# Optimization experiments

Hardware: AMD Instinct MI355X
Metric: run time of the kernel (lower is better)

Reference implementation:

```python
import jax, jax.numpy as jnp
import numpy as np

BLOCK = 256
H, D = 16, 128          # num_attention_heads, head_dim
HID = 2048              # hidden_size (= H*D)
FFN = 2048              # intermediate_size
E, TOPK = 8, 2          # num_local_experts, num_experts_per_tok
EPS_LN = 1e-5           # rms_norm_eps for layer norms
EPS_ATTN = float(np.finfo(np.float32).eps)  # torch RMSNorm default eps


def rmsnorm(x, w, eps):
    v = jnp.mean(jnp.square(x), axis=-1, keepdims=True)
    return x * jax.lax.rsqrt(v + eps) * w


def lightning_attn(x, slope, qkv_w, gate_w, norm_w, out_w):
    # x: [B,N,HID]; slope: [H,1,1]
    B, N, _ = x.shape
    qkv = jax.nn.silu(x @ qkv_w.T).reshape(B, N, H, 3 * D)
    q, k, v = jnp.split(qkv, 3, axis=-1)
    q = q.transpose(0, 2, 1, 3)  # [B,H,N,D]
    k = k.transpose(0, 2, 1, 3)
    v = v.transpose(0, 2, 1, 3)

    NB = N // BLOCK
    ar = jnp.arange(BLOCK, dtype=jnp.float32) + 1.0
    q_decay = jnp.exp(-slope * ar[:, None])             # [H,BLOCK,1]
    k_decay = jnp.exp(-slope * (BLOCK - ar[:, None]))   # [H,BLOCK,1]
    idx = ar[:, None] - ar[None, :]                      # [BLOCK,BLOCK]
    diag_decay = jnp.exp(jnp.where(idx >= 0, -(slope * idx), -jnp.inf))  # [H,BLOCK,BLOCK]
    block_decay = jnp.exp(-slope * BLOCK)                # [H,1,1]

    qb = q.reshape(B, H, NB, BLOCK, D).transpose(2, 0, 1, 3, 4)  # [NB,B,H,BLOCK,D]
    kb = k.reshape(B, H, NB, BLOCK, D).transpose(2, 0, 1, 3, 4)
    vb = v.reshape(B, H, NB, BLOCK, D).transpose(2, 0, 1, 3, 4)

    def step(kv, blk):
        qi, ki, vi = blk                                   # [B,H,BLOCK,D]
        o_nd = jnp.einsum('bhmd,bhde->bhme', qi * q_decay, kv)
        qk = jnp.einsum('bhmd,bhnd->bhmn', qi, ki) * diag_decay[None]
        o_d = jnp.einsum('bhmn,bhne->bhme', qk, vi)
        kv = block_decay * kv + jnp.einsum('bhmd,bhme->bhde', ki * k_decay, vi)
        return kv, o_nd + o_d

    kv0 = jnp.zeros((B, H, D, D), jnp.float32)
    _, out = jax.lax.scan(step, kv0, (qb, kb, vb))         # out: [NB,B,H,BLOCK,D]
    out = out.transpose(1, 2, 0, 3, 4).reshape(B, H, N, D)
    out = out.transpose(0, 2, 1, 3).reshape(B, N, H * D)   # b h n d -> b n (h d)
    out = rmsnorm(out, norm_w, EPS_ATTN)
    out = jax.nn.sigmoid(x @ gate_w.T) * out
    return out @ out_w.T


def moe(x, router_w, w1, w2, w3):
    # x: [B,N,HID]
    B, N, _ = x.shape
    xt = x.reshape(B * N, HID)                             # [T,HID]
    T = B * N
    logits = xt @ router_w.T                               # [T,E]
    probs = jax.nn.softmax(logits.astype(jnp.float32), axis=-1)
    w, sel = jax.lax.top_k(probs, TOPK)                    # [T,TOPK]
    w = w / jnp.sum(w, axis=-1, keepdims=True)
    w = w.astype(xt.dtype)
    # dense combine weights [T,E] (top-k experts are distinct)
    cw = jnp.zeros((T, E), xt.dtype).at[jnp.arange(T)[:, None], sel].add(w)
    h1 = jax.nn.silu(jnp.einsum('td,efd->tef', xt, w1))    # [T,E,FFN]
    h3 = jnp.einsum('td,efd->tef', xt, w3)
    ye = jnp.einsum('tef,edf->ted', h1 * h3, w2)           # [T,E,HID]
    out = jnp.einsum('te,ted->td', cw, ye)
    return out.reshape(B, N, HID)


def setup_inputs() -> dict:
    key = jax.random.key(0)
    ks = jax.random.split(key, 12)
    s = 0.02
    B, N = 1, 1024
    x = jax.random.normal(ks[0], (B, N, HID), jnp.float32)
    # ALiBi-like positive per-head decay rates
    slope_rate = (1.0 / (2.0 ** (8.0 * (jnp.arange(H, dtype=jnp.float32) + 1) / H))).reshape(H, 1, 1)
    return {
        'x': x,
        'slope_rate': slope_rate,
        'ln1_w': jnp.ones((HID,), jnp.float32),
        'ln2_w': jnp.ones((HID,), jnp.float32),
        'qkv_w': jax.random.normal(ks[1], (3 * H * D, HID), jnp.float32) * s,
        'ogate_w': jax.random.normal(ks[2], (H * D, HID), jnp.float32) * s,
        'anorm_w': jnp.ones((H * D,), jnp.float32),
        'aout_w': jax.random.normal(ks[3], (HID, H * D), jnp.float32) * s,
        'router_w': jax.random.normal(ks[4], (E, HID), jnp.float32) * s,
        'w1': jax.random.normal(ks[5], (E, FFN, HID), jnp.float32) * s,
        'w2': jax.random.normal(ks[6], (E, HID, FFN), jnp.float32) * s,
        'w3': jax.random.normal(ks[7], (E, FFN, HID), jnp.float32) * s,
    }


def reference(x, slope_rate, ln1_w, ln2_w, qkv_w, ogate_w, anorm_w, aout_w, router_w, w1, w2, w3):
    # pre-norm residual decoder layer (alpha=beta=1, postnorm=False, no shared MoE)
    r = x
    h = rmsnorm(x, ln1_w, EPS_LN)
    h = r + lightning_attn(h, slope_rate, qkv_w, ogate_w, anorm_w, aout_w)
    r = h
    h2 = rmsnorm(h, ln2_w, EPS_LN)
    return r + moe(h2, router_w, w1, w2, w3)
```

## Files before the change

kernel.cpp:

```cpp
#include <hip/hip_runtime.h>
#include <math.h>

#define NTOK 1024
#define NHID 2048
#define NQKV 6144
#define NHEADS 16
#define DHEAD 128
#define ABLK 256
#define NEXPERT 8
#define NFFN 2048
#define EPS_LN 1e-5f
#define EPS_ATTN 1.1920929e-7f

typedef __bf16 bf8v __attribute__((ext_vector_type(8)));
typedef __bf16 bf4v __attribute__((ext_vector_type(4)));
typedef float f4v __attribute__((ext_vector_type(4)));

static __device__ __forceinline__ f4v mfma16(bf8v a, bf8v b, f4v c) {
  return __builtin_amdgcn_mfma_f32_16x16x32_bf16(a, b, c, 0, 0, 0);
}

static __device__ __forceinline__ void gl2lds16(const float* g, float* l) {
  __builtin_amdgcn_global_load_lds(
      (const __attribute__((address_space(1))) float*)g,
      (__attribute__((address_space(3))) float*)l, 16, 0, 0);
}

__global__ __launch_bounds__(256) void rms_kernel(const float* __restrict__ in,
                                                  const float* __restrict__ w,
                                                  float* __restrict__ out,
                                                  const float* __restrict__ gate,
                                                  float* __restrict__ copy_out,
                                                  float eps) {
  const int row = blockIdx.x, tid = threadIdx.x;
  const float* p = in + (size_t)row * NHID;
  float4 v0 = *(const float4*)(p + 4 * tid);
  float4 v1 = *(const float4*)(p + 1024 + 4 * tid);
  float ss = v0.x * v0.x + v0.y * v0.y + v0.z * v0.z + v0.w * v0.w
           + v1.x * v1.x + v1.y * v1.y + v1.z * v1.z + v1.w * v1.w;
  for (int off = 32; off > 0; off >>= 1) ss += __shfl_down(ss, off);
  __shared__ float red[4];
  const int wv = tid >> 6, ln = tid & 63;
  if (ln == 0) red[wv] = ss;
  __syncthreads();
  const float tot = red[0] + red[1] + red[2] + red[3];
  const float rinv = rsqrtf(tot * (1.f / NHID) + eps);
  float4 w0 = *(const float4*)(w + 4 * tid);
  float4 w1 = *(const float4*)(w + 1024 + 4 * tid);
  float4 o0, o1;
  o0.x = v0.x * rinv * w0.x; o0.y = v0.y * rinv * w0.y;
  o0.z = v0.z * rinv * w0.z; o0.w = v0.w * rinv * w0.w;
  o1.x = v1.x * rinv * w1.x; o1.y = v1.y * rinv * w1.y;
  o1.z = v1.z * rinv * w1.z; o1.w = v1.w * rinv * w1.w;
  if (gate) {
    const float* gp = gate + (size_t)row * NHID;
    float4 g0 = *(const float4*)(gp + 4 * tid);
    float4 g1 = *(const float4*)(gp + 1024 + 4 * tid);
    o0.x *= g0.x; o0.y *= g0.y; o0.z *= g0.z; o0.w *= g0.w;
    o1.x *= g1.x; o1.y *= g1.y; o1.z *= g1.z; o1.w *= g1.w;
  }
  *(float4*)(out + (size_t)row * NHID + 4 * tid) = o0;
  *(float4*)(out + (size_t)row * NHID + 1024 + 4 * tid) = o1;
  if (copy_out) {
    *(float4*)(copy_out + (size_t)row * NHID + 4 * tid) = v0;
    *(float4*)(copy_out + (size_t)row * NHID + 1024 + 4 * tid) = v1;
  }
}

enum { GM_QKV = 0, GM_GATE = 1, GM_AOUT = 2, GM_MOE1 = 3, GM_MOE3 = 4, GM_MOE2 = 5 };

struct GArgs {
  const float* A; const float* B; float* C;
  const float* res;
  float* q_s; float* k_s; float* v_s;
  const int* perm; const int* segoff; const float* pw;
  float* outp;
  int N, K;
};

template <int MODE>
__global__ __launch_bounds__(256, 2) void gemm_bt(GArgs g) {
  const int n0 = blockIdx.x * 64;
  const int m0 = blockIdx.y * 128;
  int segbase = 0, cnt = 0x40000000, e = 0;
  if constexpr (MODE >= GM_MOE1) {
    e = blockIdx.z;
    segbase = g.segoff[e];
    cnt = g.segoff[e + 1] - segbase;
    if (m0 >= cnt) return;
  }
  const float* Bp = g.B + (size_t)e * g.N * g.K + (size_t)n0 * g.K;
  __shared__ float As[128 * 32];
  __shared__ float Bs[64 * 32];
  const int tid = threadIdx.x;
  const int w = tid >> 6, lane = tid & 63;
  const int wm = (w >> 1) * 64, wn = (w & 1) * 32;
  const int lm = lane & 15, quad = lane >> 4;
  const int lr = lane >> 3;
  const int coff = ((lane & 7) ^ lr) * 4;
  const int K = g.K;

  const float* aptr[4];
  const float* bptr[2];
#pragma unroll
  for (int qi = 0; qi < 4; qi++) {
    const int r = (w * 4 + qi) * 8 + lr;
    const int m = m0 + r;
    long grow;
    if constexpr (MODE == GM_MOE1 || MODE == GM_MOE3) {
      int mm = m < cnt ? m : cnt - 1;
      grow = g.perm[segbase + mm];
    } else if constexpr (MODE == GM_MOE2) {
      grow = segbase + (m < cnt ? m : cnt - 1);
    } else {
      grow = m;
    }
    aptr[qi] = g.A + (size_t)grow * K + coff;
  }
#pragma unroll
  for (int qi = 0; qi < 2; qi++) {
    const int r = (w * 2 + qi) * 8 + lr;
    bptr[qi] = Bp + (size_t)r * K + coff;
  }

  const f4v fz = {0.f, 0.f, 0.f, 0.f};
  f4v acc[4][2];
#pragma unroll
  for (int i = 0; i < 4; i++) {
    acc[i][0] = fz; acc[i][1] = fz;
  }

  for (int k0 = 0; k0 < K; k0 += 32) {
    __syncthreads();
#pragma unroll
    for (int qi = 0; qi < 4; qi++)
      gl2lds16(aptr[qi] + k0, &As[(w * 4 + qi) * 256]);
#pragma unroll
    for (int qi = 0; qi < 2; qi++)
      gl2lds16(bptr[qi] + k0, &Bs[(w * 2 + qi) * 256]);
    __syncthreads();
    bf8v af[4], bfv[2];
    const int sw = lm & 7;
#pragma unroll
    for (int i = 0; i < 4; i++) {
      const int ra = wm + i * 16 + lm;
      const float4 x0 = *(const float4*)&As[ra * 32 + (((quad * 2) ^ sw) << 2)];
      const float4 x1 = *(const float4*)&As[ra * 32 + (((quad * 2 + 1) ^ sw) << 2)];
      bf8v t;
      t[0] = (__bf16)x0.x; t[1] = (__bf16)x0.y; t[2] = (__bf16)x0.z; t[3] = (__bf16)x0.w;
      t[4] = (__bf16)x1.x; t[5] = (__bf16)x1.y; t[6] = (__bf16)x1.z; t[7] = (__bf16)x1.w;
      af[i] = t;
    }
#pragma unroll
    for (int j = 0; j < 2; j++) {
      const int rb = wn + j * 16 + lm;
      const float4 x0 = *(const float4*)&Bs[rb * 32 + (((quad * 2) ^ sw) << 2)];
      const float4 x1 = *(const float4*)&Bs[rb * 32 + (((quad * 2 + 1) ^ sw) << 2)];
      bf8v t;
      t[0] = (__bf16)x0.x; t[1] = (__bf16)x0.y; t[2] = (__bf16)x0.z; t[3] = (__bf16)x0.w;
      t[4] = (__bf16)x1.x; t[5] = (__bf16)x1.y; t[6] = (__bf16)x1.z; t[7] = (__bf16)x1.w;
      bfv[j] = t;
    }
#pragma unroll
    for (int i = 0; i < 4; i++)
#pragma unroll
      for (int j = 0; j < 2; j++) acc[i][j] = mfma16(af[i], bfv[j], acc[i][j]);
  }

#pragma unroll
  for (int i = 0; i < 4; i++) {
#pragma unroll
    for (int r = 0; r < 4; r++) {
      const int m = m0 + wm + i * 16 + quad * 4 + r;
      int tok = 0;
      float wgt = 0.f;
      if constexpr (MODE == GM_MOE2) {
        if (m < cnt) { tok = g.perm[segbase + m]; wgt = g.pw[segbase + m]; }
      }
#pragma unroll
      for (int j = 0; j < 2; j++) {
        const int col = n0 + wn + j * 16 + lm;
        float v = acc[i][j][r];
        if constexpr (MODE == GM_QKV) {
          v = v / (1.f + expf(-v));
          int head = col / 384;
          int rem = col - head * 384;
          int which = rem >> 7;
          int d = rem & 127;
          float* dst = which == 0 ? g.q_s : (which == 1 ? g.k_s : g.v_s);
          dst[((size_t)head * NTOK + m) * DHEAD + d] = v;
        } else if constexpr (MODE == GM_GATE) {
          g.C[(size_t)m * g.N + col] = 1.f / (1.f + expf(-v));
        } else if constexpr (MODE == GM_AOUT) {
          g.C[(size_t)m * g.N + col] = v + g.res[(size_t)m * g.N + col];
        } else if constexpr (MODE == GM_MOE1) {
          if (m < cnt) g.C[(size_t)(segbase + m) * g.N + col] = v / (1.f + expf(-v));
        } else if constexpr (MODE == GM_MOE3) {
          if (m < cnt) {
            size_t ix = (size_t)(segbase + m) * g.N + col;
            g.C[ix] = v * g.res[ix];
          }
        } else if constexpr (MODE == GM_MOE2) {
          if (m < cnt) atomicAdd(&g.outp[(size_t)tok * NHID + col], wgt * v);
        }
      }
    }
  }
}

__global__ __launch_bounds__(512) void attn_pass1(const float* __restrict__ k_s,
                                                  const float* __restrict__ v_s,
                                                  const float* __restrict__ slope,
                                                  float* __restrict__ S) {
  const int h = blockIdx.x >> 2, b = blockIdx.x & 3;
  const float s = slope[h];
  __shared__ __bf16 kT[128][40] __attribute__((aligned(16)));
  __shared__ __bf16 vT[128][40] __attribute__((aligned(16)));
  const int tid = threadIdx.x, wave = tid >> 6, lane = tid & 63;
  const int lm = lane & 15, quad = lane >> 4;
  const float* kb = k_s + ((size_t)h * NTOK + b * ABLK) * DHEAD;
  const float* vb = v_s + ((size_t)h * NTOK + b * ABLK) * DHEAD;
  const int sd = tid & 127, sg = (tid >> 7) * 8;
  const f4v fz = {0.f, 0.f, 0.f, 0.f};
  f4v acc[8];
#pragma unroll
  for (int j = 0; j < 8; j++) acc[j] = fz;
  for (int ic = 0; ic < 8; ic++) {
    __syncthreads();
    bf8v kq, vq;
#pragma unroll
    for (int ii = 0; ii < 8; ii++) {
      int ig = ic * 32 + sg + ii;
      float kd = expf(-s * (float)(ABLK - 1 - ig));
      kq[ii] = (__bf16)(kb[(size_t)ig * DHEAD + sd] * kd);
      vq[ii] = (__bf16)(vb[(size_t)ig * DHEAD + sd]);
    }
    *(bf8v*)&kT[sd][sg] = kq;
    *(bf8v*)&vT[sd][sg] = vq;
    __syncthreads();
    bf8v a = *(const bf8v*)&kT[wave * 16 + lm][quad * 8];
#pragma unroll
    for (int j = 0; j < 8; j++) {
      bf8v bb = *(const bf8v*)&vT[j * 16 + lm][quad * 8];
      acc[j] = mfma16(a, bb, acc[j]);
    }
  }
  float* Sp = S + (size_t)(h * 4 + b) * (128 * 128);
#pragma unroll
  for (int j = 0; j < 8; j++)
#pragma unroll
    for (int r = 0; r < 4; r++)
      Sp[(size_t)(wave * 16 + quad * 4 + r) * 128 + j * 16 + lm] = acc[j][r];
}

__global__ __launch_bounds__(512) void attn_pass2(const float* __restrict__ q_s,
                                                  const float* __restrict__ k_s,
                                                  const float* __restrict__ v_s,
                                                  const float* __restrict__ slope,
                                                  const float* __restrict__ S,
                                                  float* __restrict__ attn_raw) {
  const int h = blockIdx.x >> 2, b = blockIdx.x & 3;
  const float s = slope[h];
  __shared__ __bf16 kvb[128][136] __attribute__((aligned(16)));
  __shared__ __bf16 vT[128][40] __attribute__((aligned(16)));
  __shared__ __bf16 ki[32][136] __attribute__((aligned(16)));
  __shared__ __bf16 qkb[256][40] __attribute__((aligned(16)));
  const int tid = threadIdx.x, w = tid >> 6, lane = tid & 63;
  const int lm = lane & 15, quad = lane >> 4;
  {
    const int sd = tid >> 2;
    const int e0 = (tid & 3) * 32;
    float vals[32];
#pragma unroll
    for (int u = 0; u < 32; u++) vals[u] = 0.f;
    for (int j = 0; j < b; j++) {
      float c = expf(-s * 256.f * (float)(b - 1 - j));
      const float* Sp = S + (size_t)(h * 4 + j) * (128 * 128) + (size_t)sd * 128 + e0;
#pragma unroll
      for (int u4 = 0; u4 < 8; u4++) {
        float4 sv = *(const float4*)(Sp + u4 * 4);
        vals[u4 * 4 + 0] += c * sv.x; vals[u4 * 4 + 1] += c * sv.y;
        vals[u4 * 4 + 2] += c * sv.z; vals[u4 * 4 + 3] += c * sv.w;
      }
    }
#pragma unroll
    for (int u = 0; u < 32; u++) kvb[e0 + u][sd] = (__bf16)vals[u];
  }
  __syncthreads();
  const float* qb = q_s + ((size_t)h * NTOK + b * ABLK) * DHEAD;
  const float* kb = k_s + ((size_t)h * NTOK + b * ABLK) * DHEAD;
  const float* vb = v_s + ((size_t)h * NTOK + b * ABLK) * DHEAD;
  bf8v aq[2][4];
#pragma unroll
  for (int mf = 0; mf < 2; mf++) {
    const int m = w * 32 + mf * 16 + lm;
#pragma unroll
    for (int kc = 0; kc < 4; kc++) {
      const float* pp = qb + (size_t)m * DHEAD + kc * 32 + quad * 8;
      float4 u0 = *(const float4*)pp;
      float4 u1 = *(const float4*)(pp + 4);
      bf8v t;
      t[0] = (__bf16)u0.x; t[1] = (__bf16)u0.y; t[2] = (__bf16)u0.z; t[3] = (__bf16)u0.w;
      t[4] = (__bf16)u1.x; t[5] = (__bf16)u1.y; t[6] = (__bf16)u1.z; t[7] = (__bf16)u1.w;
      aq[mf][kc] = t;
    }
  }
  const f4v fz = {0.f, 0.f, 0.f, 0.f};
  f4v accO[2][8];
#pragma unroll
  for (int mf = 0; mf < 2; mf++)
#pragma unroll
    for (int nf = 0; nf < 8; nf++) accO[mf][nf] = fz;
#pragma unroll
  for (int kc = 0; kc < 4; kc++) {
#pragma unroll
    for (int nf = 0; nf < 8; nf++) {
      bf8v bb = *(const bf8v*)&kvb[nf * 16 + lm][kc * 32 + quad * 8];
      accO[0][nf] = mfma16(aq[0][kc], bb, accO[0][nf]);
      accO[1][nf] = mfma16(aq[1][kc], bb, accO[1][nf]);
    }
  }
#pragma unroll
  for (int mf = 0; mf < 2; mf++) {
#pragma unroll
    for (int r = 0; r < 4; r++) {
      const int m = w * 32 + mf * 16 + quad * 4 + r;
      const float qd = expf(-s * (float)(m + 1));
#pragma unroll
      for (int nf = 0; nf < 8; nf++) accO[mf][nf][r] *= qd;
    }
  }
  for (int ic = 0; ic < 8; ic++) {
    __syncthreads();
    {
      const int si = tid >> 4, dc = (tid & 15) * 8;
      const float* pp = kb + (size_t)(ic * 32 + si) * DHEAD + dc;
      float4 u0 = *(const float4*)pp;
      float4 u1 = *(const float4*)(pp + 4);
      bf8v t;
      t[0] = (__bf16)u0.x; t[1] = (__bf16)u0.y; t[2] = (__bf16)u0.z; t[3] = (__bf16)u0.w;
      t[4] = (__bf16)u1.x; t[5] = (__bf16)u1.y; t[6] = (__bf16)u1.z; t[7] = (__bf16)u1.w;
      *(bf8v*)&ki[si][dc] = t;
    }
    {
      const int se = tid & 127, sg = (tid >> 7) * 8;
      bf8v t;
#pragma unroll
      for (int ii = 0; ii < 8; ii++)
        t[ii] = (__bf16)vb[(size_t)(ic * 32 + sg + ii) * DHEAD + se];
      *(bf8v*)&vT[se][sg] = t;
    }
    __syncthreads();
    f4v acc2[2][2];
    acc2[0][0] = fz; acc2[0][1] = fz; acc2[1][0] = fz; acc2[1][1] = fz;
#pragma unroll
    for (int kc = 0; kc < 4; kc++) {
#pragma unroll
      for (int f = 0; f < 2; f++) {
        bf8v bk = *(const bf8v*)&ki[f * 16 + lm][kc * 32 + quad * 8];
        acc2[0][f] = mfma16(aq[0][kc], bk, acc2[0][f]);
        acc2[1][f] = mfma16(aq[1][kc], bk, acc2[1][f]);
      }
    }
#pragma unroll
    for (int mf = 0; mf < 2; mf++) {
#pragma unroll
      for (int f = 0; f < 2; f++) {
#pragma unroll
        for (int r = 0; r < 4; r++) {
          const int m = w * 32 + mf * 16 + quad * 4 + r;
          const int i = ic * 32 + f * 16 + lm;
          float v = acc2[mf][f][r];
          v = (m >= i) ? v * expf(-s * (float)(m - i)) : 0.f;
          qkb[m][f * 16 + lm] = (__bf16)v;
        }
      }
    }
    __syncthreads();
#pragma unroll
    for (int mf = 0; mf < 2; mf++) {
      bf8v aqk = *(const bf8v*)&qkb[w * 32 + mf * 16 + lm][quad * 8];
#pragma unroll
      for (int nf = 0; nf < 8; nf++) {
        bf8v bv = *(const bf8v*)&vT[nf * 16 + lm][quad * 8];
        accO[mf][nf] = mfma16(aqk, bv, accO[mf][nf]);
      }
    }
  }
  float* op = attn_raw + (size_t)(b * ABLK) * NHID + h * DHEAD;
#pragma unroll
  for (int mf = 0; mf < 2; mf++)
#pragma unroll
    for (int r = 0; r < 4; r++) {
      const int m = w * 32 + mf * 16 + quad * 4 + r;
#pragma unroll
      for (int nf = 0; nf < 8; nf++)
        op[(size_t)m * NHID + nf * 16 + lm] = accO[mf][nf][r];
    }
}

__global__ __launch_bounds__(256) void router_kernel(const float* __restrict__ h2,
                                                     const float* __restrict__ rw,
                                                     int* __restrict__ eidx,
                                                     float* __restrict__ ew) {
  const int wave = threadIdx.x >> 6, lane = threadIdx.x & 63;
  const int t = blockIdx.x * 4 + wave;
  float a[8];
#pragma unroll
  for (int e = 0; e < 8; e++) a[e] = 0.f;
  for (int d = lane; d < NHID; d += 64) {
    float xv = h2[(size_t)t * NHID + d];
#pragma unroll
    for (int e = 0; e < 8; e++) a[e] += xv * rw[(size_t)e * NHID + d];
  }
#pragma unroll
  for (int e = 0; e < 8; e++)
    for (int off = 32; off > 0; off >>= 1) a[e] += __shfl_down(a[e], off);
  if (lane == 0) {
    int i1 = 0;
#pragma unroll
    for (int e = 1; e < 8; e++)
      if (a[e] > a[i1]) i1 = e;
    int i2 = i1 == 0 ? 1 : 0;
#pragma unroll
    for (int e = 0; e < 8; e++) {
      if (e == i1 || e == i2) continue;
      if (a[e] > a[i2]) i2 = e;
    }
    float be = expf(a[i2] - a[i1]);
    float w1 = 1.f / (1.f + be), w2 = be / (1.f + be);
    eidx[2 * t] = i1; eidx[2 * t + 1] = i2;
    ew[2 * t] = w1; ew[2 * t + 1] = w2;
  }
}

__global__ __launch_bounds__(256) void build_lists(const int* __restrict__ eidx,
                                                   const float* __restrict__ ew,
                                                   int* __restrict__ segoff,
                                                   int* __restrict__ perm,
                                                   float* __restrict__ pw) {
  __shared__ int cnt[8], cur[8], offs[9];
  const int tid = threadIdx.x;
  if (tid < 8) cnt[tid] = 0;
  __syncthreads();
  for (int t = tid; t < NTOK; t += 256) {
    atomicAdd(&cnt[eidx[2 * t]], 1);
    atomicAdd(&cnt[eidx[2 * t + 1]], 1);
  }
  __syncthreads();
  if (tid == 0) {
    int o = 0;
    for (int e = 0; e < 8; e++) { offs[e] = o; o += cnt[e]; }
    offs[8] = o;
    for (int e = 0; e < 9; e++) segoff[e] = offs[e];
  }
  __syncthreads();
  if (tid < 8) cur[tid] = offs[tid];
  __syncthreads();
  for (int t = tid; t < NTOK; t += 256) {
    for (int k = 0; k < 2; k++) {
      int e = eidx[2 * t + k];
      int pos = atomicAdd(&cur[e], 1);
      perm[pos] = t;
      pw[pos] = ew[2 * t + k];
    }
  }
}

extern "C" void kernel_launch(void* const* d_in, const int* in_sizes, int n_in,
                              void* d_out, int out_size, void* d_ws, size_t ws_size,
                              hipStream_t stream) {
  (void)in_sizes; (void)n_in; (void)out_size; (void)ws_size;
  const float* x        = (const float*)d_in[0];
  const float* slope    = (const float*)d_in[1];
  const float* ln1_w    = (const float*)d_in[2];
  const float* ln2_w    = (const float*)d_in[3];
  const float* qkv_w    = (const float*)d_in[4];
  const float* ogate_w  = (const float*)d_in[5];
  const float* anorm_w  = (const float*)d_in[6];
  const float* aout_w   = (const float*)d_in[7];
  const float* router_w = (const float*)d_in[8];
  const float* w1       = (const float*)d_in[9];
  const float* w2       = (const float*)d_in[10];
  const float* w3       = (const float*)d_in[11];
  float* out = (float*)d_out;
  float* ws  = (float*)d_ws;

  const size_t MW = (size_t)NTOK * NHID;
  float* a_ln     = ws;
  float* q_s      = ws + MW;
  float* k_s      = ws + 2 * MW;
  float* v_s      = ws + 3 * MW;
  float* Sbuf     = ws + 4 * MW;
  float* attn_raw = ws + 4 * MW + MW / 2;
  float* gatebuf  = ws + 5 * MW + MW / 2;
  float* t1       = ws + 4 * MW + MW / 2;
  float* rbase    = ws + 6 * MW + MW / 2;
  int*   eidx   = (int*)rbase;
  float* ew     = rbase + 2048;
  int*   segoff = (int*)(rbase + 4096);
  int*   perm   = (int*)(rbase + 4112);
  float* pw     = rbase + 6160;
  float* h_res = k_s;
  float* h2    = v_s;
  float* ag    = a_ln;

  rms_kernel<<<dim3(NTOK), dim3(256), 0, stream>>>(x, ln1_w, a_ln, nullptr, nullptr, EPS_LN);
  {
    GArgs g{}; g.A = a_ln; g.B = qkv_w; g.q_s = q_s; g.k_s = k_s; g.v_s = v_s;
    g.N = NQKV; g.K = NHID;
    gemm_bt<GM_QKV><<<dim3(NQKV / 64, NTOK / 128), dim3(256), 0, stream>>>(g);
  }
  attn_pass1<<<dim3(64), dim3(512), 0, stream>>>(k_s, v_s, slope, Sbuf);
  attn_pass2<<<dim3(64), dim3(512), 0, stream>>>(q_s, k_s, v_s, slope, Sbuf, attn_raw);
  {
    GArgs g{}; g.A = a_ln; g.B = ogate_w; g.C = gatebuf; g.N = NHID; g.K = NHID;
    gemm_bt<GM_GATE><<<dim3(32, 8), dim3(256), 0, stream>>>(g);
  }
  rms_kernel<<<dim3(NTOK), dim3(256), 0, stream>>>(attn_raw, anorm_w, ag, gatebuf, nullptr, EPS_ATTN);
  {
    GArgs g{}; g.A = ag; g.B = aout_w; g.C = h_res; g.res = x; g.N = NHID; g.K = NHID;
    gemm_bt<GM_AOUT><<<dim3(32, 8), dim3(256), 0, stream>>>(g);
  }
  rms_kernel<<<dim3(NTOK), dim3(256), 0, stream>>>(h_res, ln2_w, h2, nullptr, out, EPS_LN);
  router_kernel<<<dim3(NTOK / 4), dim3(256), 0, stream>>>(h2, router_w, eidx, ew);
  build_lists<<<dim3(1), dim3(256), 0, stream>>>(eidx, ew, segoff, perm, pw);
  {
    GArgs g{}; g.A = h2; g.B = w1; g.C = t1; g.perm = perm; g.segoff = segoff;
    g.N = NFFN; g.K = NHID;
    gemm_bt<GM_MOE1><<<dim3(32, 16, 8), dim3(256), 0, stream>>>(g);
  }
  {
    GArgs g{}; g.A = h2; g.B = w3; g.C = t1; g.res = t1; g.perm = perm; g.segoff = segoff;
    g.N = NFFN; g.K = NHID;
    gemm_bt<GM_MOE3><<<dim3(32, 16, 8), dim3(256), 0, stream>>>(g);
  }
  {
    GArgs g{}; g.A = t1; g.B = w2; g.outp = out; g.perm = perm; g.segoff = segoff; g.pw = pw;
    g.N = NHID; g.K = NFFN;
    gemm_bt<GM_MOE2><<<dim3(32, 16, 8), dim3(256), 0, stream>>>(g);
  }
}
```

Measured before the change: 998.1 us.

## Double-buffer LDS tiles in gemm_bt to overlap global loads with MFMA

The GEMM main loop now uses two LDS buffers for the A and B tiles. It issues the async global-to-LDS loads for the next K-slice before converting and multiplying the current slice, and uses one barrier per iteration instead of two. Launch bounds are raised from 2 to 3 blocks per SM to allow more occupancy, which tightens the register budget and doubles the LDS footprint per block (48KB). The intent is to hide global load latency behind compute, at the risk of register spills or lower real occupancy.

```diff
diff --git a/kernel.cpp b/kernel.cpp
--- a/kernel.cpp
+++ b/kernel.cpp
@@ -79,7 +79,7 @@
 };
 
 template <int MODE>
-__global__ __launch_bounds__(256, 2) void gemm_bt(GArgs g) {
+__global__ __launch_bounds__(256, 3) void gemm_bt(GArgs g) {
   const int n0 = blockIdx.x * 64;
   const int m0 = blockIdx.y * 128;
   int segbase = 0, cnt = 0x40000000, e = 0;
@@ -90,8 +90,8 @@
     if (m0 >= cnt) return;
   }
   const float* Bp = g.B + (size_t)e * g.N * g.K + (size_t)n0 * g.K;
-  __shared__ float As[128 * 32];
-  __shared__ float Bs[64 * 32];
+  __shared__ float As[2][128 * 32];
+  __shared__ float Bs[2][64 * 32];
   const int tid = threadIdx.x;
   const int w = tid >> 6, lane = tid & 63;
   const int wm = (w >> 1) * 64, wn = (w & 1) * 32;
@@ -130,41 +130,53 @@
     acc[i][0] = fz; acc[i][1] = fz;
   }
 
-  for (int k0 = 0; k0 < K; k0 += 32) {
-    __syncthreads();
-#pragma unroll
-    for (int qi = 0; qi < 4; qi++)
-      gl2lds16(aptr[qi] + k0, &As[(w * 4 + qi) * 256]);
-#pragma unroll
-    for (int qi = 0; qi < 2; qi++)
-      gl2lds16(bptr[qi] + k0, &Bs[(w * 2 + qi) * 256]);
-    __syncthreads();
+  const int KT = K >> 5;
+#pragma unroll
+  for (int qi = 0; qi < 4; qi++) gl2lds16(aptr[qi], &As[0][(w * 4 + qi) * 256]);
+#pragma unroll
+  for (int qi = 0; qi < 2; qi++) gl2lds16(bptr[qi], &Bs[0][(w * 2 + qi) * 256]);
+  asm volatile("s_waitcnt vmcnt(0)" ::: "memory");
+  __builtin_amdgcn_s_barrier();
+
+  for (int t = 0; t < KT; ++t) {
+    const int cur = t & 1;
+    if (t + 1 < KT) {
+      const int k1 = (t + 1) << 5;
+#pragma unroll
+      for (int qi = 0; qi < 4; qi++)
+        gl2lds16(aptr[qi] + k1, &As[cur ^ 1][(w * 4 + qi) * 256]);
+#pragma unroll
+      for (int qi = 0; qi < 2; qi++)
+        gl2lds16(bptr[qi] + k1, &Bs[cur ^ 1][(w * 2 + qi) * 256]);
+    }
     bf8v af[4], bfv[2];
     const int sw = lm & 7;
 #pragma unroll
     for (int i = 0; i < 4; i++) {
       const int ra = wm + i * 16 + lm;
-      const float4 x0 = *(const float4*)&As[ra * 32 + (((quad * 2) ^ sw) << 2)];
-      const float4 x1 = *(const float4*)&As[ra * 32 + (((quad * 2 + 1) ^ sw) << 2)];
-      bf8v t;
-      t[0] = (__bf16)x0.x; t[1] = (__bf16)x0.y; t[2] = (__bf16)x0.z; t[3] = (__bf16)x0.w;
-      t[4] = (__bf16)x1.x; t[5] = (__bf16)x1.y; t[6] = (__bf16)x1.z; t[7] = (__bf16)x1.w;
-      af[i] = t;
+      const float4 x0 = *(const float4*)&As[cur][ra * 32 + (((quad * 2) ^ sw) << 2)];
+      const float4 x1 = *(const float4*)&As[cur][ra * 32 + (((quad * 2 + 1) ^ sw) << 2)];
+      bf8v t8;
+      t8[0] = (__bf16)x0.x; t8[1] = (__bf16)x0.y; t8[2] = (__bf16)x0.z; t8[3] = (__bf16)x0.w;
+      t8[4] = (__bf16)x1.x; t8[5] = (__bf16)x1.y; t8[6] = (__bf16)x1.z; t8[7] = (__bf16)x1.w;
+      af[i] = t8;
     }
 #pragma unroll
     for (int j = 0; j < 2; j++) {
       const int rb = wn + j * 16 + lm;
-      const float4 x0 = *(const float4*)&Bs[rb * 32 + (((quad * 2) ^ sw) << 2)];
-      const float4 x1 = *(const float4*)&Bs[rb * 32 + (((quad * 2 + 1) ^ sw) << 2)];
-      bf8v t;
-      t[0] = (__bf16)x0.x; t[1] = (__bf16)x0.y; t[2] = (__bf16)x0.z; t[3] = (__bf16)x0.w;
-      t[4] = (__bf16)x1.x; t[5] = (__bf16)x1.y; t[6] = (__bf16)x1.z; t[7] = (__bf16)x1.w;
-      bfv[j] = t;
+      const float4 x0 = *(const float4*)&Bs[cur][rb * 32 + (((quad * 2) ^ sw) << 2)];
+      const float4 x1 = *(const float4*)&Bs[cur][rb * 32 + (((quad * 2 + 1) ^ sw) << 2)];
+      bf8v t8;
+      t8[0] = (__bf16)x0.x; t8[1] = (__bf16)x0.y; t8[2] = (__bf16)x0.z; t8[3] = (__bf16)x0.w;
+      t8[4] = (__bf16)x1.x; t8[5] = (__bf16)x1.y; t8[6] = (__bf16)x1.z; t8[7] = (__bf16)x1.w;
+      bfv[j] = t8;
     }
 #pragma unroll
     for (int i = 0; i < 4; i++)
 #pragma unroll
       for (int j = 0; j < 2; j++) acc[i][j] = mfma16(af[i], bfv[j], acc[i][j]);
+    asm volatile("s_waitcnt vmcnt(0) lgkmcnt(0)" ::: "memory");
+    __builtin_amdgcn_s_barrier();
   }
 
 #pragma unroll
```

Result: faster. 874.8 us (-12.4%).
